# Performance work log

Hardware: AMD Instinct MI355X
Metric: run time of the kernel (lower is better)

## Reference

```python
import jax, jax.numpy as jnp
import numpy as np

B, S, H = 1, 2048, 768
NH, HD, NF = 12, 64, 128
ALPHA = 0.9
SIGMA = 1.0
EPS_NORM = 1e-5


def setup_inputs() -> dict:
    key = jax.random.key(0)
    ks = jax.random.split(key, 12)
    s = 1.0 / np.sqrt(H)
    inp = {
        "hidden_states": jax.random.normal(ks[0], (B, S, H), dtype=jnp.float32),
        "attention_mask": jnp.ones((B, 1, 1, S), dtype=jnp.float32),
        "Wq": jax.random.normal(ks[1], (H, H), dtype=jnp.float32) * s,
        "bq": jnp.zeros((H,), dtype=jnp.float32),
        "Wk": jax.random.normal(ks[2], (H, H), dtype=jnp.float32) * s,
        "bk": jnp.zeros((H,), dtype=jnp.float32),
        "Wv": jax.random.normal(ks[3], (H, H), dtype=jnp.float32) * s,
        "bv": jnp.zeros((H,), dtype=jnp.float32),
        "Wo": jax.random.normal(ks[4], (H, H), dtype=jnp.float32) * s,
        "bo": jnp.zeros((H,), dtype=jnp.float32),
        # per-head RFF params: omega ~ N(0, I), bias ~ U[0, 2pi]
        "omega": jax.random.normal(ks[5], (NH, NF, HD), dtype=jnp.float32),
        "rff_b": jax.random.uniform(ks[6], (NH, NF), dtype=jnp.float32, maxval=2.0 * np.pi),
    }
    return inp


def _phi(x, omega, rff_b):
    # x: (b, h, s, d) -> RFF features (b, h, s, f)
    z = jnp.einsum("bhsd,hfd->bhsf", x, omega) / SIGMA + rff_b[None, :, None, :]
    phi = jnp.sqrt(2.0 / NF) * jnp.cos(z)
    # normalize=True: L2-normalize feature vectors
    phi = phi / (jnp.linalg.norm(phi, axis=-1, keepdims=True) + 1e-6)
    return phi


def reference(hidden_states, attention_mask, Wq, bq, Wk, bk, Wv, bv, Wo, bo, omega, rff_b):
    b, s, _ = hidden_states.shape

    def proj(W, bias):
        y = jnp.einsum("bsh,oh->bso", hidden_states, W) + bias
        return y.reshape(b, s, NH, HD).transpose(0, 2, 1, 3)  # (b,h,s,d)

    q = proj(Wq, bq)
    k = proj(Wk, bk)
    v = proj(Wv, bv)

    dot_scores = jnp.einsum("bhsd,bhtd->bhst", q, k) / jnp.sqrt(jnp.float32(HD))

    qn = q / (jnp.linalg.norm(q, axis=-1, keepdims=True) + EPS_NORM)
    kn = k / (jnp.linalg.norm(k, axis=-1, keepdims=True) + EPS_NORM)
    phi_q = _phi(qn, omega, rff_b)
    phi_k = _phi(kn, omega, rff_b)
    kernel_scores = jnp.einsum("bhsf,bhtf->bhst", phi_q, phi_k)

    scores = ALPHA * dot_scores + (1.0 - ALPHA) * kernel_scores
    scores = scores + (attention_mask - 1.0) * 10000.0

    weights = jax.nn.softmax(scores, axis=-1)  # dropout is identity in eval
    context = jnp.einsum("bhst,bhtd->bhsd", weights, v)
    context = context.transpose(0, 2, 1, 3).reshape(b, s, H)
    output = jnp.einsum("bsh,oh->bso", context, Wo) + bo
    return output, weights
```

## Files before the change

### kernel.cpp

```cpp
#include <hip/hip_runtime.h>
#include <cmath>

#define TS 2048
#define TH 768
#define TNH 12
#define THD 64
#define TNF 128
#define KC 192

typedef __attribute__((ext_vector_type(4))) short s16x4;
typedef __attribute__((ext_vector_type(8))) short short8;
typedef __attribute__((ext_vector_type(8))) __bf16 bf16x8;
typedef __attribute__((ext_vector_type(4))) float floatx4;

__device__ __forceinline__ short f2bf(float x) {
    union { float f; unsigned u; } v; v.f = x;
    unsigned r = v.u + 0x7FFFu + ((v.u >> 16) & 1u);
    return (short)(r >> 16);
}
__device__ __forceinline__ float bf2f(short x) {
    union { unsigned u; float f; } v;
    v.u = ((unsigned)(unsigned short)x) << 16;
    return v.f;
}

__device__ __forceinline__ float waveReduceSum(float v) {
#pragma unroll
    for (int off = 32; off >= 1; off >>= 1) v += __shfl_xor(v, off, 64);
    return v;
}
__device__ __forceinline__ float waveReduceMax(float v) {
#pragma unroll
    for (int off = 32; off >= 1; off >>= 1) v = fmaxf(v, __shfl_xor(v, off, 64));
    return v;
}

__global__ __launch_bounds__(256) void k_cvt_bf16(
    const float* __restrict__ s0, const float* __restrict__ s1,
    const float* __restrict__ s2, const float* __restrict__ s3,
    const float* __restrict__ s4, const float* __restrict__ s5,
    short* __restrict__ d0, short* __restrict__ d1,
    short* __restrict__ d2, short* __restrict__ d3,
    short* __restrict__ d4, short* __restrict__ d5) {
    const int y = blockIdx.y;
    const float* srcs[6] = {s0, s1, s2, s3, s4, s5};
    short* dsts[6] = {d0, d1, d2, d3, d4, d5};
    const int n4s[6] = {TS * TH / 4, TH * TH / 4, TH * TH / 4, TH * TH / 4,
                        TH * TH / 4, TNH * TNF * THD / 4};
    const float* src = srcs[y];
    short* dst = dsts[y];
    const int n4 = n4s[y];
    for (int i = blockIdx.x * 256 + threadIdx.x; i < n4; i += gridDim.x * 256) {
        float4 v = ((const float4*)src)[i];
        s16x4 o;
        o[0] = f2bf(v.x); o[1] = f2bf(v.y); o[2] = f2bf(v.z); o[3] = f2bf(v.w);
        *(s16x4*)&dst[i * 4] = o;
    }
}

__global__ __launch_bounds__(256) void k_proj_qkv_mfma(
    const short* __restrict__ Xb,
    const short* __restrict__ Wqb, const short* __restrict__ Wkb, const short* __restrict__ Wvb,
    const float* __restrict__ b0, const float* __restrict__ b1, const float* __restrict__ b2,
    float* __restrict__ dq, float* __restrict__ dk, short* __restrict__ Vb,
    short* __restrict__ Qc, short* __restrict__ Kc) {
    __shared__ __align__(16) short Asb[128][40];
    __shared__ __align__(16) short Bsb[128][40];
    const int z = blockIdx.z;
    const short* W = (z == 0) ? Wqb : ((z == 1) ? Wkb : Wvb);
    const float* bias = (z == 0) ? b0 : ((z == 1) ? b1 : b2);
    const int n0 = blockIdx.x * 128;
    const int m0 = blockIdx.y * 128;
    const int tid = threadIdx.x;
    const int lane = tid & 63;
    const int w = tid >> 6;
    const int wm = (w >> 1) * 64, wn = (w & 1) * 64;
    const int fr = lane & 15;
    const int quad = lane >> 4;

    floatx4 acc[4][4] = {};

    for (int k0 = 0; k0 < TH; k0 += 32) {
#pragma unroll
        for (int l = 0; l < 2; ++l) {
            int c = tid + l * 256;
            int row = c >> 2, col = (c & 3) << 3;
            *(short8*)&Asb[row][col] = *(const short8*)&Xb[(size_t)(m0 + row) * TH + k0 + col];
            *(short8*)&Bsb[row][col] = *(const short8*)&W[(size_t)(n0 + row) * TH + k0 + col];
        }
        __syncthreads();
        bf16x8 af[4], bfr[4];
#pragma unroll
        for (int i = 0; i < 4; ++i) af[i] = *(const bf16x8*)&Asb[wm + i * 16 + fr][quad * 8];
#pragma unroll
        for (int j = 0; j < 4; ++j) bfr[j] = *(const bf16x8*)&Bsb[wn + j * 16 + fr][quad * 8];
#pragma unroll
        for (int i = 0; i < 4; ++i)
#pragma unroll
            for (int j = 0; j < 4; ++j)
                acc[i][j] = __builtin_amdgcn_mfma_f32_16x16x32_bf16(af[i], bfr[j], acc[i][j], 0, 0, 0);
        __syncthreads();
    }
    if (z == 2) {
#pragma unroll
        for (int j = 0; j < 4; ++j) {
            int n = n0 + wn + j * 16 + fr;
            int h = n >> 6, d = n & 63;
            float bv = bias[n];
#pragma unroll
            for (int i = 0; i < 4; ++i) {
                int t = m0 + wm + i * 16 + quad * 4;
                s16x4 pk;
#pragma unroll
                for (int r = 0; r < 4; ++r) pk[r] = f2bf(acc[i][j][r] + bv);
                *(s16x4*)&Vb[(size_t)(h * THD + d) * TS + t] = pk;
            }
        }
    } else {
        float* dst = z ? dk : dq;
        short* cc = z ? Kc : Qc;
        const float qs = z ? 1.0f : 0.1125f;
#pragma unroll
        for (int j = 0; j < 4; ++j) {
            int n = n0 + wn + j * 16 + fr;
            int h = n >> 6, d = n & 63;
            float bv = bias[n];
#pragma unroll
            for (int i = 0; i < 4; ++i) {
#pragma unroll
                for (int r = 0; r < 4; ++r) {
                    int m = m0 + wm + i * 16 + quad * 4 + r;
                    float val = acc[i][j][r] + bv;
                    size_t rowi = (size_t)(h * TS + m);
                    dst[rowi * THD + d] = val;
                    cc[rowi * KC + d] = f2bf(val * qs);
                }
            }
        }
    }
}

__global__ __launch_bounds__(256) void k_proj_out_mfma(
    const short* __restrict__ ctxb, const short* __restrict__ Wob,
    const float* __restrict__ bias, float* __restrict__ out) {
    __shared__ __align__(16) short Asb[128][40];
    __shared__ __align__(16) short Bsb[128][40];
    const int n0 = blockIdx.x * 128;
    const int m0 = blockIdx.y * 128;
    const int tid = threadIdx.x;
    const int lane = tid & 63;
    const int w = tid >> 6;
    const int wm = (w >> 1) * 64, wn = (w & 1) * 64;
    const int fr = lane & 15;
    const int quad = lane >> 4;

    floatx4 acc[4][4] = {};

    for (int k0 = 0; k0 < TH; k0 += 32) {
#pragma unroll
        for (int l = 0; l < 2; ++l) {
            int c = tid + l * 256;
            int row = c >> 2, col = (c & 3) << 3;
            *(short8*)&Asb[row][col] = *(const short8*)&ctxb[(size_t)(m0 + row) * TH + k0 + col];
            *(short8*)&Bsb[row][col] = *(const short8*)&Wob[(size_t)(n0 + row) * TH + k0 + col];
        }
        __syncthreads();
        bf16x8 af[4], bfr[4];
#pragma unroll
        for (int i = 0; i < 4; ++i) af[i] = *(const bf16x8*)&Asb[wm + i * 16 + fr][quad * 8];
#pragma unroll
        for (int j = 0; j < 4; ++j) bfr[j] = *(const bf16x8*)&Bsb[wn + j * 16 + fr][quad * 8];
#pragma unroll
        for (int i = 0; i < 4; ++i)
#pragma unroll
            for (int j = 0; j < 4; ++j)
                acc[i][j] = __builtin_amdgcn_mfma_f32_16x16x32_bf16(af[i], bfr[j], acc[i][j], 0, 0, 0);
        __syncthreads();
    }
#pragma unroll
    for (int j = 0; j < 4; ++j) {
        int n = n0 + wn + j * 16 + fr;
        float bv = bias[n];
#pragma unroll
        for (int i = 0; i < 4; ++i)
#pragma unroll
            for (int r = 0; r < 4; ++r) {
                int m = m0 + wm + i * 16 + quad * 4 + r;
                out[(size_t)m * TH + n] = acc[i][j][r] + bv;
            }
    }
}

__global__ __launch_bounds__(64) void k_rownorm(
    const float* __restrict__ q, const float* __restrict__ kbuf,
    float* __restrict__ invq, float* __restrict__ invk) {
    const int row = blockIdx.x;
    const float* src = blockIdx.y ? kbuf : q;
    float* dst = blockIdx.y ? invk : invq;
    float x = src[row * THD + threadIdx.x];
    float ss = waveReduceSum(x * x);
    if (threadIdx.x == 0) dst[row] = 1.0f / (sqrtf(ss) + 1e-5f);
}

__global__ __launch_bounds__(256) void k_phi_mfma(
    const float* __restrict__ q, const float* __restrict__ kbuf,
    const float* __restrict__ invq, const float* __restrict__ invk,
    const short* __restrict__ omegab, const float* __restrict__ rffb,
    short* __restrict__ Qc, short* __restrict__ Kc) {
    __shared__ __align__(16) short Asb[128][40];
    __shared__ __align__(16) short Bsb[128][40];
    const int z = blockIdx.y;
    const int h = z >> 1, which = z & 1;
    const float* X = which ? kbuf : q;
    const float* inv = which ? invk : invq;
    short* dst = which ? Kc : Qc;
    const int m0 = blockIdx.x * 128;
    const int tid = threadIdx.x;
    const int lane = tid & 63;
    const int w = tid >> 6;
    const int wm = (w >> 1) * 64, wn = (w & 1) * 64;
    const int fr = lane & 15;
    const int quad = lane >> 4;

    floatx4 acc[4][4] = {};

    for (int k0 = 0; k0 < THD; k0 += 32) {
#pragma unroll
        for (int l = 0; l < 2; ++l) {
            int c = tid + l * 256;
            int row = c >> 2, col = (c & 3) << 3;
            int rq = h * TS + m0 + row;
            float s = inv[rq];
            float4 a0 = *(const float4*)&X[(size_t)rq * THD + k0 + col];
            float4 a1 = *(const float4*)&X[(size_t)rq * THD + k0 + col + 4];
            short8 o;
            o[0] = f2bf(a0.x * s); o[1] = f2bf(a0.y * s);
            o[2] = f2bf(a0.z * s); o[3] = f2bf(a0.w * s);
            o[4] = f2bf(a1.x * s); o[5] = f2bf(a1.y * s);
            o[6] = f2bf(a1.z * s); o[7] = f2bf(a1.w * s);
            *(short8*)&Asb[row][col] = o;
            *(short8*)&Bsb[row][col] = *(const short8*)&omegab[(size_t)(h * TNF + row) * THD + k0 + col];
        }
        __syncthreads();
        bf16x8 af[4], bfr[4];
#pragma unroll
        for (int i = 0; i < 4; ++i) af[i] = *(const bf16x8*)&Asb[wm + i * 16 + fr][quad * 8];
#pragma unroll
        for (int j = 0; j < 4; ++j) bfr[j] = *(const bf16x8*)&Bsb[wn + j * 16 + fr][quad * 8];
#pragma unroll
        for (int i = 0; i < 4; ++i)
#pragma unroll
            for (int j = 0; j < 4; ++j)
                acc[i][j] = __builtin_amdgcn_mfma_f32_16x16x32_bf16(af[i], bfr[j], acc[i][j], 0, 0, 0);
        __syncthreads();
    }
#pragma unroll
    for (int j = 0; j < 4; ++j) {
        int f = wn + j * 16 + fr;
        float bv = rffb[h * TNF + f];
#pragma unroll
        for (int i = 0; i < 4; ++i)
#pragma unroll
            for (int r = 0; r < 4; ++r) {
                int m = m0 + wm + i * 16 + quad * 4 + r;
                float zv = acc[i][j][r] + bv;
                dst[(size_t)(h * TS + m) * KC + 64 + f] = f2bf(0.125f * cosf(zv));
            }
    }
}

__global__ __launch_bounds__(128) void k_phinorm(short* __restrict__ Qc, short* __restrict__ Kc) {
    const int row = blockIdx.x;
    short* buf = (blockIdx.y ? Kc : Qc) + (size_t)row * KC + 64;
    const float scale0 = blockIdx.y ? 1.0f : 0.1f;
    const int tid = threadIdx.x;
    float p = bf2f(buf[tid]);
    float ss = waveReduceSum(p * p);
    __shared__ float sh[2];
    if ((tid & 63) == 0) sh[tid >> 6] = ss;
    __syncthreads();
    ss = sh[0] + sh[1];
    float sc = scale0 / (sqrtf(ss) + 1e-6f);
    buf[tid] = f2bf(p * sc);
}

__global__ __launch_bounds__(256) void k_scores_mfma(
    const short* __restrict__ Qc, const short* __restrict__ Kc,
    const float* __restrict__ mask, float* __restrict__ wout) {
    __shared__ __align__(16) short Asb[128][40];
    __shared__ __align__(16) short Bsb[128][40];
    const int h = blockIdx.z;
    const int n0 = blockIdx.x * 128;
    const int m0 = blockIdx.y * 128;
    const int tid = threadIdx.x;
    const int lane = tid & 63;
    const int w = tid >> 6;
    const int wm = (w >> 1) * 64, wn = (w & 1) * 64;
    const int fr = lane & 15;
    const int quad = lane >> 4;

    floatx4 acc[4][4] = {};

    for (int k0 = 0; k0 < KC; k0 += 32) {
#pragma unroll
        for (int l = 0; l < 2; ++l) {
            int c = tid + l * 256;
            int row = c >> 2, col = (c & 3) << 3;
            short8 a = *(const short8*)&Qc[(size_t)(h * TS + m0 + row) * KC + k0 + col];
            *(short8*)&Asb[row][col] = a;
            short8 b = *(const short8*)&Kc[(size_t)(h * TS + n0 + row) * KC + k0 + col];
            *(short8*)&Bsb[row][col] = b;
        }
        __syncthreads();
        bf16x8 af[4], bfr[4];
#pragma unroll
        for (int i = 0; i < 4; ++i) af[i] = *(const bf16x8*)&Asb[wm + i * 16 + fr][quad * 8];
#pragma unroll
        for (int j = 0; j < 4; ++j) bfr[j] = *(const bf16x8*)&Bsb[wn + j * 16 + fr][quad * 8];
#pragma unroll
        for (int i = 0; i < 4; ++i)
#pragma unroll
            for (int j = 0; j < 4; ++j)
                acc[i][j] = __builtin_amdgcn_mfma_f32_16x16x32_bf16(af[i], bfr[j], acc[i][j], 0, 0, 0);
        __syncthreads();
    }
#pragma unroll
    for (int j = 0; j < 4; ++j) {
        int col_g = n0 + wn + j * 16 + fr;
        float mb = (mask[col_g] - 1.0f) * 10000.0f;
#pragma unroll
        for (int i = 0; i < 4; ++i) {
#pragma unroll
            for (int r = 0; r < 4; ++r) {
                int row_g = m0 + wm + i * 16 + quad * 4 + r;
                wout[(size_t)(h * TS + row_g) * TS + col_g] = acc[i][j][r] + mb;
            }
        }
    }
}

__global__ __launch_bounds__(256) void k_softmax(float* __restrict__ wout) {
    const int row = blockIdx.x;
    float4* p = (float4*)(wout + (size_t)row * TS);
    const int tid = threadIdx.x;
    float4 x0 = p[tid], x1 = p[tid + 256];
    float mx = fmaxf(fmaxf(fmaxf(x0.x, x0.y), fmaxf(x0.z, x0.w)),
                     fmaxf(fmaxf(x1.x, x1.y), fmaxf(x1.z, x1.w)));
    mx = waveReduceMax(mx);
    __shared__ float rm[4];
    __shared__ float rs[4];
    if ((tid & 63) == 0) rm[tid >> 6] = mx;
    __syncthreads();
    mx = fmaxf(fmaxf(rm[0], rm[1]), fmaxf(rm[2], rm[3]));
    float e[8];
    e[0] = __expf(x0.x - mx); e[1] = __expf(x0.y - mx);
    e[2] = __expf(x0.z - mx); e[3] = __expf(x0.w - mx);
    e[4] = __expf(x1.x - mx); e[5] = __expf(x1.y - mx);
    e[6] = __expf(x1.z - mx); e[7] = __expf(x1.w - mx);
    float sum = ((e[0] + e[1]) + (e[2] + e[3])) + ((e[4] + e[5]) + (e[6] + e[7]));
    sum = waveReduceSum(sum);
    if ((tid & 63) == 0) rs[tid >> 6] = sum;
    __syncthreads();
    sum = rs[0] + rs[1] + rs[2] + rs[3];
    float rinv = 1.0f / sum;
    x0.x = e[0] * rinv; x0.y = e[1] * rinv; x0.z = e[2] * rinv; x0.w = e[3] * rinv;
    x1.x = e[4] * rinv; x1.y = e[5] * rinv; x1.z = e[6] * rinv; x1.w = e[7] * rinv;
    p[tid] = x0;
    p[tid + 256] = x1;
}

__global__ __launch_bounds__(256) void k_ctx_mfma(
    const float* __restrict__ wout, const short* __restrict__ Vb, short* __restrict__ ctxb) {
    __shared__ __align__(16) short Asb[128][40];
    __shared__ __align__(16) short Bsb[64][40];
    const int h = blockIdx.y;
    const int m0 = blockIdx.x * 128;
    const int tid = threadIdx.x;
    const int lane = tid & 63;
    const int w = tid >> 6;
    const int wm = w * 32;
    const int fr = lane & 15;
    const int quad = lane >> 4;
    floatx4 acc[2][4] = {};
    for (int k0 = 0; k0 < TS; k0 += 32) {
#pragma unroll
        for (int l = 0; l < 4; ++l) {
            int idx = tid + l * 256;
            int row = idx >> 3, col = (idx & 7) << 2;
            float4 a = *(const float4*)&wout[(size_t)(h * TS + m0 + row) * TS + k0 + col];
            s16x4 s;
            s[0] = f2bf(a.x); s[1] = f2bf(a.y); s[2] = f2bf(a.z); s[3] = f2bf(a.w);
            *(s16x4*)&Asb[row][col] = s;
        }
        {
            int row = tid >> 2, col = (tid & 3) << 3;
            *(short8*)&Bsb[row][col] =
                *(const short8*)&Vb[(size_t)(h * THD + row) * TS + k0 + col];
        }
        __syncthreads();
        bf16x8 af[2], bfr[4];
#pragma unroll
        for (int i = 0; i < 2; ++i) af[i] = *(const bf16x8*)&Asb[wm + i * 16 + fr][quad * 8];
#pragma unroll
        for (int j = 0; j < 4; ++j) bfr[j] = *(const bf16x8*)&Bsb[j * 16 + fr][quad * 8];
#pragma unroll
        for (int i = 0; i < 2; ++i)
#pragma unroll
            for (int j = 0; j < 4; ++j)
                acc[i][j] = __builtin_amdgcn_mfma_f32_16x16x32_bf16(af[i], bfr[j], acc[i][j], 0, 0, 0);
        __syncthreads();
    }
#pragma unroll
    for (int i = 0; i < 2; ++i)
#pragma unroll
        for (int j = 0; j < 4; ++j)
#pragma unroll
            for (int r = 0; r < 4; ++r) {
                int row_g = m0 + wm + i * 16 + quad * 4 + r;
                ctxb[(size_t)row_g * TH + h * THD + j * 16 + fr] = f2bf(acc[i][j][r]);
            }
}

extern "C" void kernel_launch(void* const* d_in, const int* in_sizes, int n_in,
                              void* d_out, int out_size, void* d_ws, size_t ws_size,
                              hipStream_t stream) {
    const float* hs    = (const float*)d_in[0];
    const float* mask  = (const float*)d_in[1];
    const float* Wq    = (const float*)d_in[2];
    const float* bq    = (const float*)d_in[3];
    const float* Wk    = (const float*)d_in[4];
    const float* bk    = (const float*)d_in[5];
    const float* Wv    = (const float*)d_in[6];
    const float* bv    = (const float*)d_in[7];
    const float* Wo    = (const float*)d_in[8];
    const float* bo    = (const float*)d_in[9];
    const float* omega = (const float*)d_in[10];
    const float* rffb  = (const float*)d_in[11];

    float* out0 = (float*)d_out;
    float* wout = out0 + TS * TH;

    float* ws   = (float*)d_ws;
    float* q    = ws;
    float* kbuf = ws + 1572864;
    short* Vb   = (short*)(ws + 3145728);
    short* Wob  = (short*)(ws + 3932160);
    short* omegab = (short*)(ws + 4227072);
    float* invq = ws + 4718592;
    float* invk = ws + 4743168;
    short* ctxb = (short*)(ws + 4767744);
    short* Qc   = (short*)(ws + 6340608);
    short* Kc   = (short*)(ws + 8699904);

    short* Xb  = (short*)wout;
    short* Wqb = Xb + (size_t)TS * TH;
    short* Wkb = Wqb + (size_t)TH * TH;
    short* Wvb = Wkb + (size_t)TH * TH;

    k_cvt_bf16<<<dim3(512, 6), 256, 0, stream>>>(hs, Wq, Wk, Wv, Wo, omega,
                                                 Xb, Wqb, Wkb, Wvb, Wob, omegab);
    k_proj_qkv_mfma<<<dim3(6, 16, 3), 256, 0, stream>>>(Xb, Wqb, Wkb, Wvb, bq, bk, bv,
                                                        q, kbuf, Vb, Qc, Kc);
    k_rownorm<<<dim3(TNH * TS, 2), 64, 0, stream>>>(q, kbuf, invq, invk);
    k_phi_mfma<<<dim3(16, 24), 256, 0, stream>>>(q, kbuf, invq, invk, omegab, rffb, Qc, Kc);
    k_phinorm<<<dim3(TNH * TS, 2), 128, 0, stream>>>(Qc, Kc);
    k_scores_mfma<<<dim3(16, 16, 12), 256, 0, stream>>>(Qc, Kc, mask, wout);
    k_softmax<<<TNH * TS, 256, 0, stream>>>(wout);
    k_ctx_mfma<<<dim3(16, 12), 256, 0, stream>>>(wout, Vb, ctxb);
    k_proj_out_mfma<<<dim3(6, 16), 256, 0, stream>>>(ctxb, Wob, bo, out0);
}
```

Measured before the change: 512.0 us.

## Fuse QK score GEMM with row softmax in a single kernel

Replaces the separate score GEMM and softmax kernels with one kernel. Each block owns 16 query rows of a head and computes all 2048 scores in registers (32 MFMA accumulators per wave), then does the max/exp/sum reduction through shuffles and shared memory before writing normalized weights once. This removes one full write and read of the 12x2048x2048 fp32 score matrix and a launch. In exchange, K tiles are reloaded for every 16-row block, which costs much more K bandwidth and lowers MFMA reuse, and register pressure is high.

```diff
diff --git a/kernel.cpp b/kernel.cpp
--- a/kernel.cpp
+++ b/kernel.cpp
@@ -27,11 +27,6 @@
 __device__ __forceinline__ float waveReduceSum(float v) {
 #pragma unroll
     for (int off = 32; off >= 1; off >>= 1) v += __shfl_xor(v, off, 64);
-    return v;
-}
-__device__ __forceinline__ float waveReduceMax(float v) {
-#pragma unroll
-    for (int off = 32; off >= 1; off >>= 1) v = fmaxf(v, __shfl_xor(v, off, 64));
     return v;
 }
 
@@ -284,89 +279,114 @@
     buf[tid] = f2bf(p * sc);
 }
 
-__global__ __launch_bounds__(256) void k_scores_mfma(
+__global__ __launch_bounds__(256) void k_qk_sm(
     const short* __restrict__ Qc, const short* __restrict__ Kc,
     const float* __restrict__ mask, float* __restrict__ wout) {
-    __shared__ __align__(16) short Asb[128][40];
-    __shared__ __align__(16) short Bsb[128][40];
-    const int h = blockIdx.z;
-    const int n0 = blockIdx.x * 128;
-    const int m0 = blockIdx.y * 128;
+    __shared__ __align__(16) short Qs[16][200];
+    __shared__ __align__(16) short Ks[128][200];
+    __shared__ float smM[4][16];
+    __shared__ float smS[4][16];
+    const int h = blockIdx.y;
+    const int m0 = blockIdx.x * 16;
     const int tid = threadIdx.x;
     const int lane = tid & 63;
     const int w = tid >> 6;
-    const int wm = (w >> 1) * 64, wn = (w & 1) * 64;
     const int fr = lane & 15;
     const int quad = lane >> 4;
 
-    floatx4 acc[4][4] = {};
-
-    for (int k0 = 0; k0 < KC; k0 += 32) {
-#pragma unroll
-        for (int l = 0; l < 2; ++l) {
-            int c = tid + l * 256;
-            int row = c >> 2, col = (c & 3) << 3;
-            short8 a = *(const short8*)&Qc[(size_t)(h * TS + m0 + row) * KC + k0 + col];
-            *(short8*)&Asb[row][col] = a;
-            short8 b = *(const short8*)&Kc[(size_t)(h * TS + n0 + row) * KC + k0 + col];
-            *(short8*)&Bsb[row][col] = b;
-        }
-        __syncthreads();
-        bf16x8 af[4], bfr[4];
-#pragma unroll
-        for (int i = 0; i < 4; ++i) af[i] = *(const bf16x8*)&Asb[wm + i * 16 + fr][quad * 8];
-#pragma unroll
-        for (int j = 0; j < 4; ++j) bfr[j] = *(const bf16x8*)&Bsb[wn + j * 16 + fr][quad * 8];
-#pragma unroll
-        for (int i = 0; i < 4; ++i)
-#pragma unroll
-            for (int j = 0; j < 4; ++j)
-                acc[i][j] = __builtin_amdgcn_mfma_f32_16x16x32_bf16(af[i], bfr[j], acc[i][j], 0, 0, 0);
-        __syncthreads();
-    }
-#pragma unroll
-    for (int j = 0; j < 4; ++j) {
-        int col_g = n0 + wn + j * 16 + fr;
+    for (int i = tid; i < 384; i += 256) {
+        int row = i / 24, p = i % 24;
+        *(short8*)&Qs[row][p * 8] = *(const short8*)&Qc[(size_t)(h * TS + m0 + row) * KC + p * 8];
+    }
+    __syncthreads();
+    bf16x8 af[6];
+#pragma unroll
+    for (int k = 0; k < 6; ++k) af[k] = *(const bf16x8*)&Qs[fr][k * 32 + quad * 8];
+
+    floatx4 acc[32];
+#pragma unroll
+    for (int t = 0; t < 32; ++t) acc[t] = (floatx4){0.f, 0.f, 0.f, 0.f};
+
+#pragma unroll
+    for (int c = 0; c < 16; ++c) {
+#pragma unroll
+        for (int l = 0; l < 6; ++l) {
+            int idx = tid + l * 256;
+            int row = idx / 12, p = idx % 12;
+            *(short8*)((short*)&Ks[row][0] + p * 16) =
+                *(const short8*)&Kc[(size_t)(h * TS + c * 128 + row) * KC + p * 16];
+            *(short8*)((short*)&Ks[row][0] + p * 16 + 8) =
+                *(const short8*)&Kc[(size_t)(h * TS + c * 128 + row) * KC + p * 16 + 8];
+        }
+        __syncthreads();
+#pragma unroll
+        for (int sub = 0; sub < 2; ++sub) {
+            const int t = c * 2 + sub;
+#pragma unroll
+            for (int k = 0; k < 6; ++k) {
+                bf16x8 bf = *(const bf16x8*)&Ks[w * 32 + sub * 16 + fr][k * 32 + quad * 8];
+                acc[t] = __builtin_amdgcn_mfma_f32_16x16x32_bf16(af[k], bf, acc[t], 0, 0, 0);
+            }
+        }
+        __syncthreads();
+    }
+#pragma unroll
+    for (int t = 0; t < 32; ++t) {
+        int col_g = (t >> 1) * 128 + w * 32 + (t & 1) * 16 + fr;
         float mb = (mask[col_g] - 1.0f) * 10000.0f;
 #pragma unroll
-        for (int i = 0; i < 4; ++i) {
-#pragma unroll
-            for (int r = 0; r < 4; ++r) {
-                int row_g = m0 + wm + i * 16 + quad * 4 + r;
-                wout[(size_t)(h * TS + row_g) * TS + col_g] = acc[i][j][r] + mb;
-            }
-        }
-    }
-}
-
-__global__ __launch_bounds__(256) void k_softmax(float* __restrict__ wout) {
-    const int row = blockIdx.x;
-    float4* p = (float4*)(wout + (size_t)row * TS);
-    const int tid = threadIdx.x;
-    float4 x0 = p[tid], x1 = p[tid + 256];
-    float mx = fmaxf(fmaxf(fmaxf(x0.x, x0.y), fmaxf(x0.z, x0.w)),
-                     fmaxf(fmaxf(x1.x, x1.y), fmaxf(x1.z, x1.w)));
-    mx = waveReduceMax(mx);
-    __shared__ float rm[4];
-    __shared__ float rs[4];
-    if ((tid & 63) == 0) rm[tid >> 6] = mx;
+        for (int r = 0; r < 4; ++r) acc[t][r] += mb;
+    }
+    float m4[4];
+#pragma unroll
+    for (int r = 0; r < 4; ++r) {
+        float m = acc[0][r];
+#pragma unroll
+        for (int t = 1; t < 32; ++t) m = fmaxf(m, acc[t][r]);
+#pragma unroll
+        for (int off = 1; off <= 8; off <<= 1) m = fmaxf(m, __shfl_xor(m, off, 64));
+        m4[r] = m;
+    }
+    if (fr == 0) {
+#pragma unroll
+        for (int r = 0; r < 4; ++r) smM[w][quad * 4 + r] = m4[r];
+    }
     __syncthreads();
-    mx = fmaxf(fmaxf(rm[0], rm[1]), fmaxf(rm[2], rm[3]));
-    float e[8];
-    e[0] = __expf(x0.x - mx); e[1] = __expf(x0.y - mx);
-    e[2] = __expf(x0.z - mx); e[3] = __expf(x0.w - mx);
-    e[4] = __expf(x1.x - mx); e[5] = __expf(x1.y - mx);
-    e[6] = __expf(x1.z - mx); e[7] = __expf(x1.w - mx);
-    float sum = ((e[0] + e[1]) + (e[2] + e[3])) + ((e[4] + e[5]) + (e[6] + e[7]));
-    sum = waveReduceSum(sum);
-    if ((tid & 63) == 0) rs[tid >> 6] = sum;
+#pragma unroll
+    for (int r = 0; r < 4; ++r)
+        m4[r] = fmaxf(fmaxf(smM[0][quad * 4 + r], smM[1][quad * 4 + r]),
+                      fmaxf(smM[2][quad * 4 + r], smM[3][quad * 4 + r]));
+    float s4[4] = {0.f, 0.f, 0.f, 0.f};
+#pragma unroll
+    for (int t = 0; t < 32; ++t)
+#pragma unroll
+        for (int r = 0; r < 4; ++r) {
+            float e = __expf(acc[t][r] - m4[r]);
+            acc[t][r] = e;
+            s4[r] += e;
+        }
+#pragma unroll
+    for (int r = 0; r < 4; ++r)
+#pragma unroll
+        for (int off = 1; off <= 8; off <<= 1) s4[r] += __shfl_xor(s4[r], off, 64);
+    if (fr == 0) {
+#pragma unroll
+        for (int r = 0; r < 4; ++r) smS[w][quad * 4 + r] = s4[r];
+    }
     __syncthreads();
-    sum = rs[0] + rs[1] + rs[2] + rs[3];
-    float rinv = 1.0f / sum;
-    x0.x = e[0] * rinv; x0.y = e[1] * rinv; x0.z = e[2] * rinv; x0.w = e[3] * rinv;
-    x1.x = e[4] * rinv; x1.y = e[5] * rinv; x1.z = e[6] * rinv; x1.w = e[7] * rinv;
-    p[tid] = x0;
-    p[tid + 256] = x1;
+#pragma unroll
+    for (int r = 0; r < 4; ++r) {
+        float s = smS[0][quad * 4 + r] + smS[1][quad * 4 + r] +
+                  smS[2][quad * 4 + r] + smS[3][quad * 4 + r];
+        s4[r] = 1.0f / s;
+    }
+#pragma unroll
+    for (int t = 0; t < 32; ++t) {
+        int col_g = (t >> 1) * 128 + w * 32 + (t & 1) * 16 + fr;
+#pragma unroll
+        for (int r = 0; r < 4; ++r)
+            wout[(size_t)(h * TS + m0 + quad * 4 + r) * TS + col_g] = acc[t][r] * s4[r];
+    }
 }
 
 __global__ __launch_bounds__(256) void k_ctx_mfma(
@@ -464,8 +484,7 @@
     k_rownorm<<<dim3(TNH * TS, 2), 64, 0, stream>>>(q, kbuf, invq, invk);
     k_phi_mfma<<<dim3(16, 24), 256, 0, stream>>>(q, kbuf, invq, invk, omegab, rffb, Qc, Kc);
     k_phinorm<<<dim3(TNH * TS, 2), 128, 0, stream>>>(Qc, Kc);
-    k_scores_mfma<<<dim3(16, 16, 12), 256, 0, stream>>>(Qc, Kc, mask, wout);
-    k_softmax<<<TNH * TS, 256, 0, stream>>>(wout);
+    k_qk_sm<<<dim3(TS / 16, TNH), 256, 0, stream>>>(Qc, Kc, mask, wout);
     k_ctx_mfma<<<dim3(16, 12), 256, 0, stream>>>(wout, Vb, ctxb);
     k_proj_out_mfma<<<dim3(6, 16), 256, 0, stream>>>(ctxb, Wob, bo, out0);
 }
```

New measurement: 558.8 us. 1.09x slower.

## Fuse row norms into QKV projection and phi normalization into phi kernel

Applied to the files above, without the earlier changes.

The QKV projection epilogue now computes per-row sums of squares through lane shuffles and writes the inverse norms directly. It no longer stores fp32 Q/K, and the separate rownorm kernel is removed. The phi kernel reads the bf16 Q/K already stored in Qc/Kc, rescaling by inv/qs, and L2-normalizes the cosine features in-block through shared-memory partial sums, which removes the phinorm kernel. This saves two launches and the fp32 round trips, at the cost of phi inputs coming from a bf16-rounded copy.

```diff
diff --git a/kernel.cpp b/kernel.cpp
--- a/kernel.cpp
+++ b/kernel.cpp
@@ -62,7 +62,7 @@
     const short* __restrict__ Xb,
     const short* __restrict__ Wqb, const short* __restrict__ Wkb, const short* __restrict__ Wvb,
     const float* __restrict__ b0, const float* __restrict__ b1, const float* __restrict__ b2,
-    float* __restrict__ dq, float* __restrict__ dk, short* __restrict__ Vb,
+    float* __restrict__ invq, float* __restrict__ invk, short* __restrict__ Vb,
     short* __restrict__ Qc, short* __restrict__ Kc) {
     __shared__ __align__(16) short Asb[128][40];
     __shared__ __align__(16) short Bsb[128][40];
@@ -117,13 +117,15 @@
             }
         }
     } else {
-        float* dst = z ? dk : dq;
         short* cc = z ? Kc : Qc;
+        float* invd = z ? invk : invq;
         const float qs = z ? 1.0f : 0.1125f;
+        const int hh = (n0 + wn) >> 6;
+        float ssr[4][4] = {};
 #pragma unroll
         for (int j = 0; j < 4; ++j) {
             int n = n0 + wn + j * 16 + fr;
-            int h = n >> 6, d = n & 63;
+            int d = n & 63;
             float bv = bias[n];
 #pragma unroll
             for (int i = 0; i < 4; ++i) {
@@ -131,12 +133,23 @@
                 for (int r = 0; r < 4; ++r) {
                     int m = m0 + wm + i * 16 + quad * 4 + r;
                     float val = acc[i][j][r] + bv;
-                    size_t rowi = (size_t)(h * TS + m);
-                    dst[rowi * THD + d] = val;
-                    cc[rowi * KC + d] = f2bf(val * qs);
+                    cc[(size_t)(hh * TS + m) * KC + d] = f2bf(val * qs);
+                    ssr[i][r] += val * val;
                 }
             }
         }
+#pragma unroll
+        for (int i = 0; i < 4; ++i)
+#pragma unroll
+            for (int r = 0; r < 4; ++r) {
+                float ss = ssr[i][r];
+#pragma unroll
+                for (int off = 1; off <= 8; off <<= 1) ss += __shfl_xor(ss, off, 64);
+                if (fr == 0) {
+                    int m = m0 + wm + i * 16 + quad * 4 + r;
+                    invd[hh * TS + m] = 1.0f / (qs * (sqrtf(ss) + 1e-5f));
+                }
+            }
     }
 }
 
@@ -191,29 +204,17 @@
     }
 }
 
-__global__ __launch_bounds__(64) void k_rownorm(
-    const float* __restrict__ q, const float* __restrict__ kbuf,
-    float* __restrict__ invq, float* __restrict__ invk) {
-    const int row = blockIdx.x;
-    const float* src = blockIdx.y ? kbuf : q;
-    float* dst = blockIdx.y ? invk : invq;
-    float x = src[row * THD + threadIdx.x];
-    float ss = waveReduceSum(x * x);
-    if (threadIdx.x == 0) dst[row] = 1.0f / (sqrtf(ss) + 1e-5f);
-}
-
 __global__ __launch_bounds__(256) void k_phi_mfma(
-    const float* __restrict__ q, const float* __restrict__ kbuf,
     const float* __restrict__ invq, const float* __restrict__ invk,
     const short* __restrict__ omegab, const float* __restrict__ rffb,
     short* __restrict__ Qc, short* __restrict__ Kc) {
     __shared__ __align__(16) short Asb[128][40];
     __shared__ __align__(16) short Bsb[128][40];
+    __shared__ float smP[4][64];
     const int z = blockIdx.y;
     const int h = z >> 1, which = z & 1;
-    const float* X = which ? kbuf : q;
     const float* inv = which ? invk : invq;
-    short* dst = which ? Kc : Qc;
+    short* buf = which ? Kc : Qc;
     const int m0 = blockIdx.x * 128;
     const int tid = threadIdx.x;
     const int lane = tid & 63;
@@ -231,13 +232,10 @@
             int row = c >> 2, col = (c & 3) << 3;
             int rq = h * TS + m0 + row;
             float s = inv[rq];
-            float4 a0 = *(const float4*)&X[(size_t)rq * THD + k0 + col];
-            float4 a1 = *(const float4*)&X[(size_t)rq * THD + k0 + col + 4];
+            short8 a = *(const short8*)&buf[(size_t)rq * KC + k0 + col];
             short8 o;
-            o[0] = f2bf(a0.x * s); o[1] = f2bf(a0.y * s);
-            o[2] = f2bf(a0.z * s); o[3] = f2bf(a0.w * s);
-            o[4] = f2bf(a1.x * s); o[5] = f2bf(a1.y * s);
-            o[6] = f2bf(a1.z * s); o[7] = f2bf(a1.w * s);
+#pragma unroll
+            for (int e = 0; e < 8; ++e) o[e] = f2bf(bf2f(a[e]) * s);
             *(short8*)&Asb[row][col] = o;
             *(short8*)&Bsb[row][col] = *(const short8*)&omegab[(size_t)(h * TNF + row) * THD + k0 + col];
         }
@@ -254,34 +252,49 @@
                 acc[i][j] = __builtin_amdgcn_mfma_f32_16x16x32_bf16(af[i], bfr[j], acc[i][j], 0, 0, 0);
         __syncthreads();
     }
-#pragma unroll
-    for (int j = 0; j < 4; ++j) {
-        int f = wn + j * 16 + fr;
-        float bv = rffb[h * TNF + f];
-#pragma unroll
-        for (int i = 0; i < 4; ++i)
+    float bvj[4];
+#pragma unroll
+    for (int j = 0; j < 4; ++j) bvj[j] = rffb[h * TNF + wn + j * 16 + fr];
+    float ssr[4][4] = {};
+#pragma unroll
+    for (int i = 0; i < 4; ++i)
+#pragma unroll
+        for (int j = 0; j < 4; ++j)
 #pragma unroll
             for (int r = 0; r < 4; ++r) {
-                int m = m0 + wm + i * 16 + quad * 4 + r;
-                float zv = acc[i][j][r] + bv;
-                dst[(size_t)(h * TS + m) * KC + 64 + f] = f2bf(0.125f * cosf(zv));
-            }
-    }
-}
-
-__global__ __launch_bounds__(128) void k_phinorm(short* __restrict__ Qc, short* __restrict__ Kc) {
-    const int row = blockIdx.x;
-    short* buf = (blockIdx.y ? Kc : Qc) + (size_t)row * KC + 64;
-    const float scale0 = blockIdx.y ? 1.0f : 0.1f;
-    const int tid = threadIdx.x;
-    float p = bf2f(buf[tid]);
-    float ss = waveReduceSum(p * p);
-    __shared__ float sh[2];
-    if ((tid & 63) == 0) sh[tid >> 6] = ss;
+                float p = 0.125f * cosf(acc[i][j][r] + bvj[j]);
+                acc[i][j][r] = p;
+                ssr[i][r] += p * p;
+            }
+#pragma unroll
+    for (int i = 0; i < 4; ++i)
+#pragma unroll
+        for (int r = 0; r < 4; ++r) {
+#pragma unroll
+            for (int off = 1; off <= 8; off <<= 1) ssr[i][r] += __shfl_xor(ssr[i][r], off, 64);
+        }
+    if (fr == 0) {
+#pragma unroll
+        for (int i = 0; i < 4; ++i)
+#pragma unroll
+            for (int r = 0; r < 4; ++r) smP[w][i * 16 + quad * 4 + r] = ssr[i][r];
+    }
     __syncthreads();
-    ss = sh[0] + sh[1];
-    float sc = scale0 / (sqrtf(ss) + 1e-6f);
-    buf[tid] = f2bf(p * sc);
+    const float scale0 = which ? 1.0f : 0.1f;
+#pragma unroll
+    for (int i = 0; i < 4; ++i)
+#pragma unroll
+        for (int r = 0; r < 4; ++r) {
+            int rl = i * 16 + quad * 4 + r;
+            float ss = smP[w][rl] + smP[w ^ 1][rl];
+            float sc = scale0 / (sqrtf(ss) + 1e-6f);
+            int m = m0 + wm + rl;
+#pragma unroll
+            for (int j = 0; j < 4; ++j) {
+                int f = wn + j * 16 + fr;
+                buf[(size_t)(h * TS + m) * KC + 64 + f] = f2bf(acc[i][j][r] * sc);
+            }
+        }
 }
 
 __global__ __launch_bounds__(256) void k_scores_mfma(
@@ -441,8 +454,6 @@
     float* wout = out0 + TS * TH;
 
     float* ws   = (float*)d_ws;
-    float* q    = ws;
-    float* kbuf = ws + 1572864;
     short* Vb   = (short*)(ws + 3145728);
     short* Wob  = (short*)(ws + 3932160);
     short* omegab = (short*)(ws + 4227072);
@@ -460,10 +471,8 @@
     k_cvt_bf16<<<dim3(512, 6), 256, 0, stream>>>(hs, Wq, Wk, Wv, Wo, omega,
                                                  Xb, Wqb, Wkb, Wvb, Wob, omegab);
     k_proj_qkv_mfma<<<dim3(6, 16, 3), 256, 0, stream>>>(Xb, Wqb, Wkb, Wvb, bq, bk, bv,
-                                                        q, kbuf, Vb, Qc, Kc);
-    k_rownorm<<<dim3(TNH * TS, 2), 64, 0, stream>>>(q, kbuf, invq, invk);
-    k_phi_mfma<<<dim3(16, 24), 256, 0, stream>>>(q, kbuf, invq, invk, omegab, rffb, Qc, Kc);
-    k_phinorm<<<dim3(TNH * TS, 2), 128, 0, stream>>>(Qc, Kc);
+                                                        invq, invk, Vb, Qc, Kc);
+    k_phi_mfma<<<dim3(16, 24), 256, 0, stream>>>(invq, invk, omegab, rffb, Qc, Kc);
     k_scores_mfma<<<dim3(16, 16, 12), 256, 0, stream>>>(Qc, Kc, mask, wout);
     k_softmax<<<TNH * TS, 256, 0, stream>>>(wout);
     k_ctx_mfma<<<dim3(16, 12), 256, 0, stream>>>(wout, Vb, ctxb);
```

Result: faster. 489.0 us (-4.5%).
